# Performance work log

Hardware: AMD Instinct MI355X
Metric: run time of the kernel (lower is better)

Reference implementation:

```python
import jax, jax.numpy as jnp
import numpy as np

NX = 2048
NY = 2048
LINK_LEN = 100.0  # uniform link length (m)

RHO_W, RHO_I, G = 1000.0, 917.0, 9.81
SEC_PER_A = 31556926.0
K_S, A_S = 0.01, 1.25          # sheet conductivity / flow exponent
K_C, A_C = 0.1, 3.0            # channel conductivity / flow exponent
H_R, L_C = 0.1, 2.0            # bedrock step height / cavity spacing
A_CL, N_GLEN = 5e-25, 3        # closure coeff / Glen exponent
C_T, C_W = 7.5e-8, 4220.0      # pressure-melt coeff / heat capacity


def _build_grid(nx, ny):
    ids = np.arange(nx * ny, dtype=np.int32).reshape(ny, nx)
    # links: tail -> head, horizontal then vertical
    h_tail = ids[:, :-1].ravel(); h_head = ids[:, 1:].ravel()
    v_tail = ids[:-1, :].ravel(); v_head = ids[1:, :].ravel()
    tail = np.concatenate([h_tail, v_tail]); head = np.concatenate([h_head, v_head])
    adj = np.full((ny, nx, 4), -1, dtype=np.int32)
    adj[:, 1:, 0] = ids[:, :-1]   # left
    adj[:, :-1, 1] = ids[:, 1:]   # right
    adj[1:, :, 2] = ids[:-1, :]   # down
    adj[:-1, :, 3] = ids[1:, :]   # up
    status = np.zeros((ny, nx), dtype=np.int32)
    status[0, :] = status[-1, :] = 1
    status[:, 0] = status[:, -1] = 1
    return head, tail, adj.reshape(-1, 4), status.ravel()


def setup_inputs() -> dict:
    key = jax.random.key(0)
    ks = jax.random.split(key, 6)
    head, tail, adj, status = _build_grid(NX, NY)
    N = NX * NY
    L = head.shape[0]
    bedrock = jax.random.uniform(ks[0], (N,), dtype=jnp.float32) * 500.0
    ice_thickness = jax.random.uniform(ks[1], (N,), dtype=jnp.float32) * 1000.0 + 100.0
    base = RHO_W * G * bedrock
    overburden = base + RHO_I * G * ice_thickness
    potential = base + 0.8 * (overburden - base) + jax.random.normal(ks[2], (N,), dtype=jnp.float32) * 1e3
    sheet_thickness = jax.random.uniform(ks[3], (N,), dtype=jnp.float32) * 0.2
    channel_size = jax.random.uniform(ks[4], (L,), dtype=jnp.float32) * 2.0
    sliding_velocity = jax.random.normal(ks[5], (L,), dtype=jnp.float32) * 50.0  # m/a on links
    return dict(
        potential=potential,
        sheet_thickness=sheet_thickness,
        channel_size=channel_size,
        bedrock_elevation=bedrock,
        ice_thickness=ice_thickness,
        sliding_velocity=sliding_velocity,
        node_at_link_head=jnp.asarray(head),
        node_at_link_tail=jnp.asarray(tail),
        adjacent_nodes_at_node=jnp.asarray(adj),
        status_at_node=jnp.asarray(status),
    )


def reference(potential, sheet_thickness, channel_size, bedrock_elevation, ice_thickness,
              sliding_velocity, node_at_link_head, node_at_link_tail,
              adjacent_nodes_at_node, status_at_node):
    head, tail = node_at_link_head, node_at_link_tail
    n_nodes = potential.shape[0]

    base = RHO_W * G * bedrock_elevation                       # base_potential
    overburden = base + RHO_I * G * ice_thickness              # overburden_potential

    grad = (potential[head] - potential[tail]) / LINK_LEN      # calc_grad_at_link
    flow_direction = jnp.where(potential[head] > potential[tail], -1, 1)

    # set_inflow_outflow
    adj = adjacent_nodes_at_node
    max_adj = jnp.max(jnp.where(adj != -1, potential[adj], -jnp.inf), axis=1)
    boundary = (status_at_node > 0).astype(jnp.int32)
    inflow_outflow = jnp.where(potential > max_adj, boundary, -boundary)

    water_pressure = potential - base
    eff_N = overburden - potential

    # sheet / channel discharge on links
    h_link = 0.5 * (sheet_thickness[head] + sheet_thickness[tail])
    sheet_q = -K_S * h_link ** A_S * jnp.abs(grad) ** (-0.5) * grad
    channel_q = -K_C * channel_size ** A_C * grad

    # calc_sheet_opening: mean of |u_b|/sec_per_a over links at each node
    u = jnp.abs(sliding_velocity) / SEC_PER_A
    seg = jnp.concatenate([head, tail])
    val = jnp.concatenate([u, u])
    num = jax.ops.segment_sum(val, seg, num_segments=n_nodes)
    cnt = jax.ops.segment_sum(jnp.ones_like(val), seg, num_segments=n_nodes)
    sliding_node = num / jnp.maximum(cnt, 1.0)
    opening = jnp.where(sheet_thickness < H_R,
                        sliding_node * (H_R - sheet_thickness) / L_C, 0.0)

    relu = lambda x: jnp.where(x > 0.0, x, 0.0)
    sheet_closure = A_CL * sheet_thickness * relu(eff_N) ** N_GLEN
    N_link = 0.5 * (eff_N[head] + eff_N[tail])
    channel_closure = A_CL * channel_size * relu(N_link) ** N_GLEN

    dissipation = jnp.abs(channel_q * grad) + jnp.abs(L_C * sheet_q * grad)

    p_grad = (water_pressure[head] - water_pressure[tail]) / LINK_LEN
    total_q = jnp.where((channel_size > 0) | (p_grad * sheet_q > 0),
                        channel_q + L_C * sheet_q, channel_q)
    sensible = (-C_T * C_W * RHO_W) * total_q * p_grad

    return (flow_direction, inflow_outflow, sheet_q, channel_q, opening,
            sheet_closure, channel_closure, dissipation, sensible)
```

## Files before the change

kernel.cpp:

```cpp
#include <hip/hip_runtime.h>
#include <math.h>

constexpr int NXc = 2048;
constexpr int NYc = 2048;
constexpr int LH   = NYc * (NXc - 1);
constexpr int LV   = (NYc - 1) * NXc;
constexpr int LTOT = LH + LV;
constexpr int NN   = NXc * NYc;

constexpr int OFF_FDIR  = 0;
constexpr int OFF_IO    = LTOT;
constexpr int OFF_SQ    = LTOT + NN;
constexpr int OFF_CQ    = 2 * LTOT + NN;
constexpr int OFF_OPEN  = 3 * LTOT + NN;
constexpr int OFF_SCL   = 3 * LTOT + 2 * NN;
constexpr int OFF_CCL   = 3 * LTOT + 3 * NN;
constexpr int OFF_DISS  = 4 * LTOT + 3 * NN;
constexpr int OFF_SENS  = 5 * LTOT + 3 * NN;

__global__ __launch_bounds__(256) void sgd_kernel(
    const float* __restrict__ pot,
    const float* __restrict__ sheet,
    const float* __restrict__ csz,
    const float* __restrict__ bed,
    const float* __restrict__ ice,
    const float* __restrict__ sv,
    const int*   __restrict__ status,
    float* __restrict__ out)
{
    constexpr float RWG     = 9810.0f;
    constexpr float RIG     = 8996.77f;
    constexpr float LINKL   = 100.0f;
    constexpr float KS      = 0.01f;
    constexpr float KC      = 0.1f;
    constexpr float ACL     = 5e-25f;
    constexpr float SEC_A   = 31556926.0f;
    constexpr float SENS_C  = 0.3165f;

    const int idx = blockIdx.x * 256 + threadIdx.x;

    if (idx < LTOT) {
        int ht, hh;
        if (idx < LH) {
            int y = idx / (NXc - 1);
            int x = idx - y * (NXc - 1);
            ht = y * NXc + x;
            hh = ht + 1;
        } else {
            ht = idx - LH;
            hh = ht + NXc;
        }

        const float pt = pot[ht],   ph = pot[hh];
        const float st = sheet[ht], sh = sheet[hh];
        const float bt = bed[ht],   bh = bed[hh];
        const float it = ice[ht],   ih = ice[hh];
        const float cs = csz[idx];

        const float grad = (ph - pt) / LINKL;
        const float fdir = (ph > pt) ? -1.0f : 1.0f;

        const float base_t = RWG * bt,            base_h = RWG * bh;
        const float ob_t   = base_t + RIG * it,   ob_h   = base_h + RIG * ih;
        const float wp_t   = pt - base_t,         wp_h   = ph - base_h;
        const float eN_t   = ob_t - pt,           eN_h   = ob_h - ph;

        const float hl = 0.5f * (sh + st);
        const float ag = fabsf(grad);
        const float sq = -KS * powf(hl, 1.25f) * (grad / sqrtf(ag));
        const float cq = -KC * (cs * cs * cs) * grad;

        const float Nl  = 0.5f * (eN_h + eN_t);
        const float rc  = fmaxf(Nl, 0.0f);
        const float ccl = ACL * cs * (rc * rc * rc);

        const float diss = fabsf(cq * grad) + fabsf(2.0f * sq * grad);

        const float pg = (wp_h - wp_t) / LINKL;
        const float tq = ((cs > 0.0f) || (pg * sq > 0.0f)) ? (cq + 2.0f * sq) : cq;
        const float sens = -SENS_C * tq * pg;

        out[OFF_FDIR + idx] = fdir;
        out[OFF_SQ   + idx] = sq;
        out[OFF_CQ   + idx] = cq;
        out[OFF_CCL  + idx] = ccl;
        out[OFF_DISS + idx] = diss;
        out[OFF_SENS + idx] = sens;
    } else if (idx < LTOT + NN) {
        const int n = idx - LTOT;
        const int y = n >> 11;
        const int x = n & (NXc - 1);

        const float p = pot[n];
        float mx = -INFINITY;
        if (x > 0)       mx = fmaxf(mx, pot[n - 1]);
        if (x < NXc - 1) mx = fmaxf(mx, pot[n + 1]);
        if (y > 0)       mx = fmaxf(mx, pot[n - NXc]);
        if (y < NYc - 1) mx = fmaxf(mx, pot[n + NXc]);

        const float bfl = (status[n] > 0) ? 1.0f : 0.0f;
        const float io  = (p > mx) ? bfl : -bfl;

        float usum = 0.0f, cnt = 0.0f;
        if (x > 0)       { usum += fabsf(sv[y * (NXc - 1) + (x - 1)]) / SEC_A; cnt += 1.0f; }
        if (x < NXc - 1) { usum += fabsf(sv[y * (NXc - 1) + x])       / SEC_A; cnt += 1.0f; }
        if (y > 0)       { usum += fabsf(sv[LH + n - NXc])            / SEC_A; cnt += 1.0f; }
        if (y < NYc - 1) { usum += fabsf(sv[LH + n])                  / SEC_A; cnt += 1.0f; }
        const float snode = usum / cnt;

        const float sh_n = sheet[n];
        const float opening = (sh_n < 0.1f) ? (snode * (0.1f - sh_n) / 2.0f) : 0.0f;

        const float eN = (RWG * bed[n] + RIG * ice[n]) - p;
        const float r  = fmaxf(eN, 0.0f);
        const float scl = ACL * sh_n * (r * r * r);

        out[OFF_IO   + n] = io;
        out[OFF_OPEN + n] = opening;
        out[OFF_SCL  + n] = scl;
    }
}

extern "C" void kernel_launch(void* const* d_in, const int* in_sizes, int n_in,
                              void* d_out, int out_size, void* d_ws, size_t ws_size,
                              hipStream_t stream) {
    const float* pot    = (const float*)d_in[0];
    const float* sheet  = (const float*)d_in[1];
    const float* csz    = (const float*)d_in[2];
    const float* bed    = (const float*)d_in[3];
    const float* ice    = (const float*)d_in[4];
    const float* sv     = (const float*)d_in[5];
    const int*   status = (const int*)d_in[9];
    float* out = (float*)d_out;

    const int total  = LTOT + NN;
    const int blocks = (total + 255) / 256;
    sgd_kernel<<<blocks, 256, 0, stream>>>(pot, sheet, csz, bed, ice, sv, status, out);
}
```

Baseline: 463.0 us.

## Swizzle blocks across XCDs, use nontemporal memory ops, cheapen sheet-flux math

Remaps block indices so that each of the eight XCDs processes a contiguous range of links and nodes, so neighbouring-node reads stay within one L2. Streaming loads and all output stores become nontemporal to reduce cache pollution. powf(h, 1.25) and the divide by sqrt become sqrt(sqrt) and rsqrt, and divides become multiplies. The tail bounds check is dropped because the total size is an exact multiple of 256. The ice-overburden constant is also corrected to 917*9.81, and rsqrt/sqrt may differ slightly in precision from the original expressions.

```diff
diff --git a/kernel.cpp b/kernel.cpp
--- a/kernel.cpp
+++ b/kernel.cpp
@@ -28,16 +28,19 @@
     const int*   __restrict__ status,
     float* __restrict__ out)
 {
-    constexpr float RWG     = 9810.0f;
-    constexpr float RIG     = 8996.77f;
-    constexpr float LINKL   = 100.0f;
-    constexpr float KS      = 0.01f;
-    constexpr float KC      = 0.1f;
-    constexpr float ACL     = 5e-25f;
-    constexpr float SEC_A   = 31556926.0f;
-    constexpr float SENS_C  = 0.3165f;
+    constexpr float RWG    = 9810.0f;
+    constexpr float RIG    = 8995.77f;
+    constexpr float INV_L  = 0.01f;
+    constexpr float KS     = 0.01f;
+    constexpr float KC     = 0.1f;
+    constexpr float ACL    = 5e-25f;
+    constexpr float SEC_A  = 31556926.0f;
+    constexpr float SENS_C = 0.3165f;
 
-    const int idx = blockIdx.x * 256 + threadIdx.x;
+    const int wg    = blockIdx.x;
+    const int chunk = (int)gridDim.x >> 3;
+    const int swz   = (wg & 7) * chunk + (wg >> 3);
+    const int idx   = swz * 256 + (int)threadIdx.x;
 
     if (idx < LTOT) {
         int ht, hh;
@@ -55,9 +58,9 @@
         const float st = sheet[ht], sh = sheet[hh];
         const float bt = bed[ht],   bh = bed[hh];
         const float it = ice[ht],   ih = ice[hh];
-        const float cs = csz[idx];
+        const float cs = __builtin_nontemporal_load(&csz[idx]);
 
-        const float grad = (ph - pt) / LINKL;
+        const float grad = (ph - pt) * INV_L;
         const float fdir = (ph > pt) ? -1.0f : 1.0f;
 
         const float base_t = RWG * bt,            base_h = RWG * bh;
@@ -67,7 +70,8 @@
 
         const float hl = 0.5f * (sh + st);
         const float ag = fabsf(grad);
-        const float sq = -KS * powf(hl, 1.25f) * (grad / sqrtf(ag));
+        const float hp = hl * sqrtf(sqrtf(hl));
+        const float sq = -KS * hp * (grad * rsqrtf(ag));
         const float cq = -KC * (cs * cs * cs) * grad;
 
         const float Nl  = 0.5f * (eN_h + eN_t);
@@ -76,17 +80,17 @@
 
         const float diss = fabsf(cq * grad) + fabsf(2.0f * sq * grad);
 
-        const float pg = (wp_h - wp_t) / LINKL;
+        const float pg = (wp_h - wp_t) * INV_L;
         const float tq = ((cs > 0.0f) || (pg * sq > 0.0f)) ? (cq + 2.0f * sq) : cq;
         const float sens = -SENS_C * tq * pg;
 
-        out[OFF_FDIR + idx] = fdir;
-        out[OFF_SQ   + idx] = sq;
-        out[OFF_CQ   + idx] = cq;
-        out[OFF_CCL  + idx] = ccl;
-        out[OFF_DISS + idx] = diss;
-        out[OFF_SENS + idx] = sens;
-    } else if (idx < LTOT + NN) {
+        __builtin_nontemporal_store(fdir, &out[OFF_FDIR + idx]);
+        __builtin_nontemporal_store(sq,   &out[OFF_SQ   + idx]);
+        __builtin_nontemporal_store(cq,   &out[OFF_CQ   + idx]);
+        __builtin_nontemporal_store(ccl,  &out[OFF_CCL  + idx]);
+        __builtin_nontemporal_store(diss, &out[OFF_DISS + idx]);
+        __builtin_nontemporal_store(sens, &out[OFF_SENS + idx]);
+    } else {
         const int n = idx - LTOT;
         const int y = n >> 11;
         const int x = n & (NXc - 1);
@@ -98,7 +102,8 @@
         if (y > 0)       mx = fmaxf(mx, pot[n - NXc]);
         if (y < NYc - 1) mx = fmaxf(mx, pot[n + NXc]);
 
-        const float bfl = (status[n] > 0) ? 1.0f : 0.0f;
+        const int  st_n = __builtin_nontemporal_load(&status[n]);
+        const float bfl = (st_n > 0) ? 1.0f : 0.0f;
         const float io  = (p > mx) ? bfl : -bfl;
 
         float usum = 0.0f, cnt = 0.0f;
@@ -109,15 +114,15 @@
         const float snode = usum / cnt;
 
         const float sh_n = sheet[n];
-        const float opening = (sh_n < 0.1f) ? (snode * (0.1f - sh_n) / 2.0f) : 0.0f;
+        const float opening = (sh_n < 0.1f) ? (snode * (0.1f - sh_n) * 0.5f) : 0.0f;
 
         const float eN = (RWG * bed[n] + RIG * ice[n]) - p;
         const float r  = fmaxf(eN, 0.0f);
         const float scl = ACL * sh_n * (r * r * r);
 
-        out[OFF_IO   + n] = io;
-        out[OFF_OPEN + n] = opening;
-        out[OFF_SCL  + n] = scl;
+        __builtin_nontemporal_store(io,      &out[OFF_IO   + n]);
+        __builtin_nontemporal_store(opening, &out[OFF_OPEN + n]);
+        __builtin_nontemporal_store(scl,     &out[OFF_SCL  + n]);
     }
 }
 
@@ -134,6 +139,6 @@
     float* out = (float*)d_out;
 
     const int total  = LTOT + NN;
-    const int blocks = (total + 255) / 256;
+    const int blocks = total / 256;
     sgd_kernel<<<blocks, 256, 0, stream>>>(pot, sheet, csz, bed, ice, sv, status, out);
 }
```

Result: slower. 509.0 us (+9.9%).
